# Performance work log

Measured on AMD Instinct MI355X. Metric: run time of the kernel, lower is better.

Reference implementation:

```python
import jax, jax.numpy as jnp
import numpy as np

B, T, D = 1, 8192, 1024
H, DH = 16, 64
WIN = 128          # attention window (tokens on each side)
WB = 128
NB = T // WB
EPS = 1e-5


def _layernorm(x, g, b):
    mu = jnp.mean(x, axis=-1, keepdims=True)
    var = jnp.mean(jnp.square(x - mu), axis=-1, keepdims=True)
    return (x - mu) * jax.lax.rsqrt(var + EPS) * g + b


def _band_mask():
    # query offset i in [0, WB), key offset j in [0, 3*WB) within [prev|self|next] blocks
    i = jnp.arange(WB)[:, None]
    j = jnp.arange(3 * WB)[None, :]
    rel = j - WB - i                      # key_pos - query_pos
    band = jnp.abs(rel) <= WIN            # sliding window |i-j| <= W (matches torch mask)
    blk = jnp.arange(NB)[:, None, None]
    key_pos = blk * WB + (j - WB)[None]   # absolute key position
    return band[None] & (key_pos >= 0) & (key_pos < T)   # [NB, WB, 3*WB]


def _local_attention(q, k, v):
    # q,k,v: [B,H,T,DH] -> block-local SDPA, mathematically identical to
    # full SDPA with the additive band mask in the torch code.
    def blocks(t):
        return t.reshape(B, H, NB, WB, DH)
    qb = blocks(q)
    kp = jnp.pad(blocks(k), ((0, 0), (0, 0), (1, 1), (0, 0), (0, 0)))
    vp = jnp.pad(blocks(v), ((0, 0), (0, 0), (1, 1), (0, 0), (0, 0)))
    # gather [prev, self, next] key/value blocks: [B,H,NB,3*WB,DH]
    k3 = jnp.concatenate([kp[:, :, s:s + NB] for s in range(3)], axis=3)
    v3 = jnp.concatenate([vp[:, :, s:s + NB] for s in range(3)], axis=3)
    scores = jnp.einsum('bhnqd,bhnkd->bhnqk', qb, k3) / np.sqrt(DH).astype(np.float32)
    mask = _band_mask()                                   # [NB,WB,3WB]
    scores = jnp.where(mask[None, None], scores, -jnp.inf)
    attn = jax.nn.softmax(scores, axis=-1)
    out = jnp.einsum('bhnqk,bhnkd->bhnqd', attn, v3)      # [B,H,NB,WB,DH]
    return out.reshape(B, H, T, DH)


def setup_inputs() -> dict:
    key = jax.random.key(0)
    ks = jax.random.split(key, 7)
    s = 0.02
    return {
        'x': jax.random.normal(ks[0], (B, T, D), jnp.float32),
        'wq': jax.random.normal(ks[1], (D, D), jnp.float32) * s,
        'wk': jax.random.normal(ks[2], (D, D), jnp.float32) * s,
        'wv': jax.random.normal(ks[3], (D, D), jnp.float32) * s,
        'wo': jax.random.normal(ks[4], (D, D), jnp.float32) * s,
        'wg': jax.random.normal(ks[5], (D, 2 * D), jnp.float32) * s,
        'wd': jax.random.normal(ks[6], (2 * D, D), jnp.float32) * s,
        'norm_g': jnp.ones((D,), jnp.float32),
        'norm_b': jnp.zeros((D,), jnp.float32),
        'ffn_g': jnp.ones((D,), jnp.float32),
        'ffn_b': jnp.zeros((D,), jnp.float32),
    }


def reference(x, wq, wk, wv, wo, wg, wd, norm_g, norm_b, ffn_g, ffn_b):
    h = _layernorm(x, norm_g, norm_b)
    def heads(t):  # [B,T,D] -> [B,H,T,DH]
        return t.reshape(B, T, H, DH).transpose(0, 2, 1, 3)
    q, k, v = heads(h @ wq), heads(h @ wk), heads(h @ wv)
    attn_out = _local_attention(q, k, v)                     # [B,H,T,DH]
    attn_out = attn_out.transpose(0, 2, 1, 3).reshape(B, T, D)
    x = x + attn_out @ wo
    h = _layernorm(x, ffn_g, ffn_b)
    x = x + jax.nn.silu(h @ wg) @ wd
    return x
```

## Files before the change

kernel.cpp:

```cpp
#include <hip/hip_runtime.h>
#include <cstdint>

#define T_DIM 8192
#define D_DIM 1024
#define NB_DIM 64
#define QKS 2048

typedef __bf16 bf16x8 __attribute__((ext_vector_type(8)));
typedef __bf16 bf16x4 __attribute__((ext_vector_type(4)));
typedef float f32x4 __attribute__((ext_vector_type(4)));

#define MFMA16(a, b, c) __builtin_amdgcn_mfma_f32_16x16x32_bf16((a), (b), (c), 0, 0, 0)
#define BAR() asm volatile("s_barrier" ::: "memory")
#define VMCNT(n) asm volatile("s_waitcnt vmcnt(" #n ")" ::: "memory")

__device__ __forceinline__ void gld_lds16(const void* gsrc, void* ldst) {
  __builtin_amdgcn_global_load_lds(
      (__attribute__((address_space(1))) void*)(uintptr_t)gsrc,
      (__attribute__((address_space(3))) void*)(uintptr_t)ldst,
      16, 0, 0);
}

__global__ __launch_bounds__(256) void prep_all(
    const float* __restrict__ wq, const float* __restrict__ wk,
    const float* __restrict__ wv, const float* __restrict__ wo,
    const float* __restrict__ wg, const float* __restrict__ wd,
    __bf16* __restrict__ wqkT, __bf16* __restrict__ wvT,
    __bf16* __restrict__ woT, __bf16* __restrict__ wgT,
    __bf16* __restrict__ wdT,
    const float* __restrict__ x, const float* __restrict__ ng,
    const float* __restrict__ nb, __bf16* __restrict__ h) {
  __shared__ float smem_f[32 * 33];
  const int bid = (int)blockIdx.x;
  const int tid = threadIdx.x;

  if (bid < 8192) {
    float (*tile)[33] = (float(*)[33])smem_f;
    const float* W; __bf16* Wt; int K, N, n0, k0, local;
    if (bid < 1024)      { W = wq; Wt = wqkT;            K = 1024; N = 1024; local = bid; }
    else if (bid < 2048) { W = wk; Wt = wqkT + 1048576;  K = 1024; N = 1024; local = bid - 1024; }
    else if (bid < 3072) { W = wv; Wt = wvT;             K = 1024; N = 1024; local = bid - 2048; }
    else if (bid < 4096) { W = wo; Wt = woT;             K = 1024; N = 1024; local = bid - 3072; }
    else if (bid < 6144) { W = wg; Wt = wgT;             K = 1024; N = 2048; local = bid - 4096; }
    else                 { W = wd; Wt = wdT;             K = 2048; N = 1024; local = bid - 6144; }
    if (N == 2048) { n0 = (local & 63) * 32; k0 = (local >> 6) * 32; }
    else           { n0 = (local & 31) * 32; k0 = (local >> 5) * 32; }
    const int tx = tid & 31, ty = tid >> 5;
#pragma unroll
    for (int i = 0; i < 32; i += 8)
      tile[ty + i][tx] = W[(size_t)(k0 + ty + i) * N + n0 + tx];
    __syncthreads();
#pragma unroll
    for (int i = 0; i < 32; i += 8)
      Wt[(size_t)(n0 + ty + i) * K + k0 + tx] = (__bf16)tile[tx][ty + i];
  } else {
    float* red = smem_f;
    const int row = bid - 8192;
    const float4 v = ((const float4*)(x + (size_t)row * D_DIM))[tid];
    float s = v.x + v.y + v.z + v.w;
#pragma unroll
    for (int off = 32; off >= 1; off >>= 1) s += __shfl_xor(s, off, 64);
    if ((tid & 63) == 0) red[tid >> 6] = s;
    __syncthreads();
    const float mean = (red[0] + red[1] + red[2] + red[3]) * (1.0f / D_DIM);
    const float d0 = v.x - mean, d1 = v.y - mean, d2 = v.z - mean, d3 = v.w - mean;
    float ss = d0 * d0 + d1 * d1 + d2 * d2 + d3 * d3;
#pragma unroll
    for (int off = 32; off >= 1; off >>= 1) ss += __shfl_xor(ss, off, 64);
    if ((tid & 63) == 0) red[4 + (tid >> 6)] = ss;
    __syncthreads();
    const float var = (red[4] + red[5] + red[6] + red[7]) * (1.0f / D_DIM);
    const float rstd = rsqrtf(var + 1e-5f);
    const float4 gg = ((const float4*)ng)[tid];
    const float4 bb = ((const float4*)nb)[tid];
    bf16x4 o;
    o[0] = (__bf16)(d0 * rstd * gg.x + bb.x);
    o[1] = (__bf16)(d1 * rstd * gg.y + bb.y);
    o[2] = (__bf16)(d2 * rstd * gg.z + bb.z);
    o[3] = (__bf16)(d3 * rstd * gg.w + bb.w);
    *(bf16x4*)(h + (size_t)row * D_DIM + tid * 4) = o;
  }
}

__global__ __launch_bounds__(256) void ln_kernel(
    const __bf16* __restrict__ x, const float* __restrict__ g,
    const float* __restrict__ b, __bf16* __restrict__ out) {
  __shared__ float red[8];
  const int row = blockIdx.x, tid = threadIdx.x;
  const bf16x4 v = ((const bf16x4*)(x + (size_t)row * D_DIM))[tid];
  const float v0 = (float)v[0], v1 = (float)v[1], v2 = (float)v[2], v3 = (float)v[3];
  float s = v0 + v1 + v2 + v3;
#pragma unroll
  for (int off = 32; off >= 1; off >>= 1) s += __shfl_xor(s, off, 64);
  if ((tid & 63) == 0) red[tid >> 6] = s;
  __syncthreads();
  const float mean = (red[0] + red[1] + red[2] + red[3]) * (1.0f / D_DIM);
  const float d0 = v0 - mean, d1 = v1 - mean, d2 = v2 - mean, d3 = v3 - mean;
  float ss = d0 * d0 + d1 * d1 + d2 * d2 + d3 * d3;
#pragma unroll
  for (int off = 32; off >= 1; off >>= 1) ss += __shfl_xor(ss, off, 64);
  if ((tid & 63) == 0) red[4 + (tid >> 6)] = ss;
  __syncthreads();
  const float var = (red[4] + red[5] + red[6] + red[7]) * (1.0f / D_DIM);
  const float rstd = rsqrtf(var + 1e-5f);
  const float4 gg = ((const float4*)g)[tid];
  const float4 bb = ((const float4*)b)[tid];
  bf16x4 o;
  o[0] = (__bf16)(d0 * rstd * gg.x + bb.x);
  o[1] = (__bf16)(d1 * rstd * gg.y + bb.y);
  o[2] = (__bf16)(d2 * rstd * gg.z + bb.z);
  o[3] = (__bf16)(d3 * rstd * gg.w + bb.w);
  *(bf16x4*)(out + (size_t)row * D_DIM + tid * 4) = o;
}

template <int BM_, int EPI, bool DUAL>
__global__ __launch_bounds__(512, 2) void gemm8(
    const __bf16* Ap, const __bf16* Btp, const void* Res, void* Coutp,
    int Mp, int Np, int K, int nbnp, int split,
    const __bf16* A2, const __bf16* Bt2, void* Cout2,
    int M2, int N2, int nbn2) {
  constexpr int MF = BM_ / 32;
  constexpr int MH = MF / 2;
  constexpr int SA = 8 * MF;
  constexpr int LA = BM_ / 128;
  constexpr int ATILE = BM_ * 64;
  constexpr int AHALF = BM_ * 32;
  constexpr int BOFF = 2 * ATILE;
  __shared__ __bf16 lds[2 * BM_ * 64 + 32768];

  const __bf16* A = Ap;
  const __bf16* Bt = Btp;
  void* Cout = Coutp;
  int M = Mp, N = Np, nbn = nbnp;
  int bid = (int)blockIdx.x;
  int nwg = gridDim.x;
  if constexpr (DUAL) {
    if (bid >= split) {
      A = A2; Bt = Bt2; Cout = Cout2; M = M2; N = N2; nbn = nbn2;
      bid -= split; nwg = gridDim.x - split;
    } else {
      nwg = split;
    }
  }
  (void)M;

  const int tid = threadIdx.x;
  const int l = tid & 63, w = tid >> 6;
  const int lr = l & 15, lg = l >> 4;
  const int wr = w >> 2, wc = w & 3;
  const int swz = (bid & 7) * (nwg >> 3) + (bid >> 3);
  const int bm = swz / nbn, bn = swz % nbn;
  const int am0 = bm * BM_, bn0 = bn * 256;

  f32x4 acc[MF][4];
  const f32x4 z4 = {0.f, 0.f, 0.f, 0.f};
#pragma unroll
  for (int m = 0; m < MF; ++m)
#pragma unroll
    for (int n = 0; n < 4; ++n) acc[m][n] = z4;

  auto stageA = [&](int h, int b, int k0) {
#pragma unroll
    for (int r = 0; r < LA; ++r) {
      const int ci = r * 512 + tid;
      const int wri = ci >> 3, c8 = ci & 7;
      const int ra = (wri % SA) + (wri / SA) * (2 * SA) + h * SA;
      gld_lds16(A + (size_t)(am0 + ra) * K + k0 + ((c8 ^ (wri & 7)) << 3),
                (__bf16*)lds + b * ATILE + h * AHALF + ci * 8);
    }
  };
  auto stageB = [&](int h, int b, int k0) {
#pragma unroll
    for (int r = 0; r < 2; ++r) {
      const int ci = r * 512 + tid;
      const int wri = ci >> 3, c8 = ci & 7;
      const int rb = (wri & 31) + (wri >> 5) * 64 + h * 32;
      gld_lds16(Bt + (size_t)(bn0 + rb) * K + k0 + ((c8 ^ (wri & 7)) << 3),
                (__bf16*)lds + BOFF + b * 16384 + h * 8192 + ci * 8);
    }
  };

  const int x7 = lr & 7;
  const int aoff0 = (lr + wr * SA) * 64 + ((lg) ^ x7) * 8;
  const int aoff1 = (lr + wr * SA) * 64 + ((4 + lg) ^ x7) * 8;
  const int boff0 = BOFF + (lr + wc * 32) * 64 + ((lg) ^ x7) * 8;
  const int boff1 = BOFF + (lr + wc * 32) * 64 + ((4 + lg) ^ x7) * 8;

  const int nt = K >> 6;
  stageA(0, 0, 0);
  stageB(1, 0, 0);
  stageB(0, 0, 0);
  stageA(1, 0, 0);
  stageA(0, 1, 64);
  stageB(1, 1, 64);
  if constexpr (BM_ == 256) VMCNT(6); else VMCNT(4);
  BAR();

  int buf = 0;
  bf16x8 afr[MH][2], bfr0[2][2], bfr1[2][2];
  for (int t = 0; t < nt; ++t) {
    const bool s1 = (t + 1 < nt);
    const bool s2 = (t + 2 < nt);
    const int nb_ = buf ^ 1;
    const int k1 = (t + 1) << 6;
    const int k2 = (t + 2) << 6;
    const __bf16* pa0 = lds + buf * ATILE + aoff0;
    const __bf16* pa1 = lds + buf * ATILE + aoff1;
    const __bf16* pb0 = lds + buf * 16384 + boff0;
    const __bf16* pb1 = lds + buf * 16384 + boff1;

#pragma unroll
    for (int i = 0; i < MH; ++i) {
      afr[i][0] = *(const bf16x8*)(pa0 + i * 1024);
      afr[i][1] = *(const bf16x8*)(pa1 + i * 1024);
    }
#pragma unroll
    for (int j = 0; j < 2; ++j) {
      bfr0[j][0] = *(const bf16x8*)(pb0 + j * 1024);
      bfr0[j][1] = *(const bf16x8*)(pb1 + j * 1024);
    }
    if (s1) stageB(0, nb_, k1);
    BAR();
    __builtin_amdgcn_s_setprio(1);
#pragma unroll
    for (int kk = 0; kk < 2; ++kk)
#pragma unroll
      for (int i = 0; i < MH; ++i)
#pragma unroll
        for (int j = 0; j < 2; ++j)
          acc[i][j] = MFMA16(afr[i][kk], bfr0[j][kk], acc[i][j]);
    __builtin_amdgcn_s_setprio(0);

#pragma unroll
    for (int j = 0; j < 2; ++j) {
      bfr1[j][0] = *(const bf16x8*)(pb0 + 8192 + j * 1024);
      bfr1[j][1] = *(const bf16x8*)(pb1 + 8192 + j * 1024);
    }
    if (s1) {
      stageA(1, nb_, k1);
      if constexpr (BM_ == 256) VMCNT(8); else VMCNT(6);
    } else {
      VMCNT(0);
    }
    BAR();
    __builtin_amdgcn_s_setprio(1);
#pragma unroll
    for (int kk = 0; kk < 2; ++kk)
#pragma unroll
      for (int i = 0; i < MH; ++i)
#pragma unroll
        for (int j = 0; j < 2; ++j)
          acc[i][2 + j] = MFMA16(afr[i][kk], bfr1[j][kk], acc[i][2 + j]);
    __builtin_amdgcn_s_setprio(0);

#pragma unroll
    for (int i = 0; i < MH; ++i) {
      afr[i][0] = *(const bf16x8*)(pa0 + AHALF + i * 1024);
      afr[i][1] = *(const bf16x8*)(pa1 + AHALF + i * 1024);
    }
    if (s2) stageA(0, buf, k2);
    BAR();
    __builtin_amdgcn_s_setprio(1);
#pragma unroll
    for (int kk = 0; kk < 2; ++kk)
#pragma unroll
      for (int i = 0; i < MH; ++i)
#pragma unroll
        for (int j = 0; j < 2; ++j)
          acc[MH + i][2 + j] = MFMA16(afr[i][kk], bfr1[j][kk], acc[MH + i][2 + j]);
    __builtin_amdgcn_s_setprio(0);

    if (s2) {
      stageB(1, buf, k2);
      if constexpr (BM_ == 256) VMCNT(6); else VMCNT(4);
    } else if (s1) {
      if constexpr (BM_ == 256) VMCNT(2); else VMCNT(1);
    }
    BAR();
    __builtin_amdgcn_s_setprio(1);
#pragma unroll
    for (int kk = 0; kk < 2; ++kk)
#pragma unroll
      for (int i = 0; i < MH; ++i)
#pragma unroll
        for (int j = 0; j < 2; ++j)
          acc[MH + i][j] = MFMA16(afr[i][kk], bfr0[j][kk], acc[MH + i][j]);
    __builtin_amdgcn_s_setprio(0);

    buf = nb_;
  }

  if constexpr (EPI == 5) {
    const __bf16* R = (const __bf16*)Res;
    float* O = (float*)Cout;
#pragma unroll
    for (int mf = 0; mf < MF; ++mf)
#pragma unroll
      for (int nf = 0; nf < 4; ++nf)
#pragma unroll
        for (int r = 0; r < 4; ++r) {
          const int row = am0 + wr * 2 * SA + mf * 16 + lg * 4 + r;
          const int col = bn0 + wc * 64 + nf * 16 + lr;
          const size_t idx = (size_t)row * N + col;
          O[idx] = acc[mf][nf][r] + (float)R[idx];
        }
  } else {
    __syncthreads();
    __bf16* Ct = (__bf16*)lds;
#pragma unroll
    for (int mf = 0; mf < MF; ++mf)
#pragma unroll
      for (int nf = 0; nf < 4; ++nf)
#pragma unroll
        for (int r = 0; r < 4; ++r) {
          const int rl = wr * 2 * SA + mf * 16 + lg * 4 + r;
          const int cl = wc * 64 + nf * 16 + lr;
          float v = acc[mf][nf][r];
          if constexpr (EPI == 3) v = v / (1.f + __expf(-v));
          if constexpr (EPI == 4)
            v += ((const float*)Res)[(size_t)(am0 + rl) * N + bn0 + cl];
          Ct[rl * 256 + (((cl >> 3) ^ (rl & 7)) << 3) + (cl & 7)] = (__bf16)v;
        }
    __syncthreads();
    __bf16* O = (__bf16*)Cout;
#pragma unroll
    for (int i = 0; i < BM_ / 16; ++i) {
      const int ci = i * 512 + tid;
      const int row = ci >> 5, c8 = ci & 31;
      *(bf16x8*)(O + (size_t)(am0 + row) * N + bn0 + c8 * 8) =
          *(const bf16x8*)&Ct[row * 256 + ((c8 ^ (row & 7)) << 3)];
    }
  }
}

template <int REL>
__device__ __forceinline__ void attn_tile(
    const __bf16* __restrict__ qk, const __bf16* __restrict__ vT,
    __bf16* Pw, const bf16x8 (&qf)[2][2], float (&ssum)[2][4],
    f32x4 (&o)[2][4], int kb, int h, int w, int lr, int lg) {
  const f32x4 z4 = {0.f, 0.f, 0.f, 0.f};
  const int kclo = (REL < 0) ? (w * 2) : 0;
  const int kchi = (REL > 0) ? (w * 2 + 2) : 8;

  f32x4 s[2][8];
  const __bf16* kbase = qk + (size_t)(kb * 128 + lr) * QKS + 1024 + h * 64 + lg * 8;
#pragma unroll
  for (int kc = 0; kc < 8; ++kc) {
    if (kc < kclo || kc >= kchi) continue;
    const bf16x8 k0 = *(const bf16x8*)(kbase + (size_t)kc * 16 * QKS);
    const bf16x8 k1 = *(const bf16x8*)(kbase + (size_t)kc * 16 * QKS + 32);
    s[0][kc] = MFMA16(qf[0][0], k0, z4);
    s[1][kc] = MFMA16(qf[1][0], k0, z4);
    s[0][kc] = MFMA16(qf[0][1], k1, s[0][kc]);
    s[1][kc] = MFMA16(qf[1][1], k1, s[1][kc]);
  }

#pragma unroll
  for (int m = 0; m < 2; ++m) {
#pragma unroll
    for (int r = 0; r < 4; ++r) {
      const int qi = w * 32 + m * 16 + lg * 4 + r;
      float acc_s = 0.f;
#pragma unroll
      for (int kc = 0; kc < 8; ++kc) {
        if (kc < kclo || kc >= kchi) continue;
        const int kj = kc * 16 + lr;
        float p = __expf(s[m][kc][r] * 0.125f);
        const bool valid = (REL == 0) || (REL < 0 ? (kj >= qi) : (kj <= qi));
        p = valid ? p : 0.f;
        s[m][kc][r] = p;
        acc_s += p;
      }
      ssum[m][r] += acc_s;
    }
  }

#pragma unroll
  for (int m = 0; m < 2; ++m)
#pragma unroll
    for (int kc = 0; kc < 8; ++kc) {
      if (kc < kclo || kc >= kchi) continue;
#pragma unroll
      for (int r = 0; r < 4; ++r)
        Pw[(m * 16 + lg * 4 + r) * 136 + kc * 16 + lr] = (__bf16)s[m][kc][r];
    }

  const int kslo = kclo >> 1, kshi = kchi >> 1;
  const __bf16* vbase = vT + (size_t)(h * 64 + lr) * T_DIM + kb * 128 + lg * 8;
#pragma unroll
  for (int ks = 0; ks < 4; ++ks) {
    if (ks < kslo || ks >= kshi) continue;
    bf16x8 pa[2];
#pragma unroll
    for (int m = 0; m < 2; ++m)
      pa[m] = *(const bf16x8*)&Pw[(m * 16 + lr) * 136 + ks * 32 + lg * 8];
#pragma unroll
    for (int n = 0; n < 4; ++n) {
      const bf16x8 vb = *(const bf16x8*)(vbase + (size_t)n * 16 * T_DIM + ks * 32);
      o[0][n] = MFMA16(pa[0], vb, o[0][n]);
      o[1][n] = MFMA16(pa[1], vb, o[1][n]);
    }
  }
}

__global__ __launch_bounds__(64, 2) void attn_kernel(
    const __bf16* __restrict__ qk, const __bf16* __restrict__ vT,
    __bf16* __restrict__ out) {
  __shared__ __bf16 Pw[32 * 136];

  const int l = (int)threadIdx.x;
  const int lr = l & 15, lg = l >> 4;
  const int bx = (int)blockIdx.x;
  const int swz = (bx & 7) * 512 + (bx >> 3);
  const int h = swz >> 8;
  const int blk = (swz >> 2) & 63;
  const int w = swz & 3;

  const __bf16* qbase =
      qk + (size_t)(blk * 128 + w * 32 + lr) * QKS + h * 64 + lg * 8;
  bf16x8 qf[2][2];
#pragma unroll
  for (int m = 0; m < 2; ++m)
#pragma unroll
    for (int ks = 0; ks < 2; ++ks)
      qf[m][ks] = *(const bf16x8*)(qbase + (size_t)m * 16 * QKS + ks * 32);

  bf16x8 kf0[8][2];
  {
    const __bf16* kbase =
        qk + (size_t)(blk * 128 + lr) * QKS + 1024 + h * 64 + lg * 8;
#pragma unroll
    for (int kc = 0; kc < 8; ++kc) {
      kf0[kc][0] = *(const bf16x8*)(kbase + (size_t)kc * 16 * QKS);
      kf0[kc][1] = *(const bf16x8*)(kbase + (size_t)kc * 16 * QKS + 32);
    }
  }

  const f32x4 z4 = {0.f, 0.f, 0.f, 0.f};
  float ssum[2][4];
  f32x4 o[2][4];
#pragma unroll
  for (int m = 0; m < 2; ++m) {
#pragma unroll
    for (int r = 0; r < 4; ++r) ssum[m][r] = 0.f;
#pragma unroll
    for (int n = 0; n < 4; ++n) o[m][n] = z4;
  }

  {
    f32x4 s[2][8];
#pragma unroll
    for (int kc = 0; kc < 8; ++kc) {
      s[0][kc] = MFMA16(qf[0][0], kf0[kc][0], z4);
      s[1][kc] = MFMA16(qf[1][0], kf0[kc][0], z4);
      s[0][kc] = MFMA16(qf[0][1], kf0[kc][1], s[0][kc]);
      s[1][kc] = MFMA16(qf[1][1], kf0[kc][1], s[1][kc]);
    }
#pragma unroll
    for (int m = 0; m < 2; ++m)
#pragma unroll
      for (int r = 0; r < 4; ++r) {
        float acc_s = 0.f;
#pragma unroll
        for (int kc = 0; kc < 8; ++kc) {
          const float p = __expf(s[m][kc][r] * 0.125f);
          s[m][kc][r] = p;
          acc_s += p;
        }
        ssum[m][r] += acc_s;
      }
#pragma unroll
    for (int m = 0; m < 2; ++m)
#pragma unroll
      for (int kc = 0; kc < 8; ++kc)
#pragma unroll
        for (int r = 0; r < 4; ++r)
          Pw[(m * 16 + lg * 4 + r) * 136 + kc * 16 + lr] = (__bf16)s[m][kc][r];
    const __bf16* vbase =
        vT + (size_t)(h * 64 + lr) * T_DIM + blk * 128 + lg * 8;
#pragma unroll
    for (int ks = 0; ks < 4; ++ks) {
      bf16x8 pa[2];
#pragma unroll
      for (int m = 0; m < 2; ++m)
        pa[m] = *(const bf16x8*)&Pw[(m * 16 + lr) * 136 + ks * 32 + lg * 8];
#pragma unroll
      for (int n = 0; n < 4; ++n) {
        const bf16x8 vb = *(const bf16x8*)(vbase + (size_t)n * 16 * T_DIM + ks * 32);
        o[0][n] = MFMA16(pa[0], vb, o[0][n]);
        o[1][n] = MFMA16(pa[1], vb, o[1][n]);
      }
    }
  }

  if (blk > 0)
    attn_tile<-1>(qk, vT, Pw, qf, ssum, o, blk - 1, h, w, lr, lg);
  if (blk < NB_DIM - 1)
    attn_tile<1>(qk, vT, Pw, qf, ssum, o, blk + 1, h, w, lr, lg);

  float inv[2][4];
#pragma unroll
  for (int m = 0; m < 2; ++m)
#pragma unroll
    for (int r = 0; r < 4; ++r) {
      float rs = ssum[m][r];
#pragma unroll
      for (int off = 1; off < 16; off <<= 1) rs += __shfl_xor(rs, off, 64);
      inv[m][r] = __builtin_amdgcn_rcpf(rs);
    }
#pragma unroll
  for (int m = 0; m < 2; ++m)
#pragma unroll
    for (int n = 0; n < 4; ++n)
#pragma unroll
      for (int r = 0; r < 4; ++r)
        Pw[(m * 16 + lg * 4 + r) * 136 + n * 16 + lr] =
            (__bf16)(o[m][n][r] * inv[m][r]);
#pragma unroll
  for (int i = 0; i < 4; ++i) {
    const int ci = i * 64 + l;
    const int qrow = ci >> 3;
    const int c8 = (ci & 7) * 8;
    const bf16x8 vv = *(const bf16x8*)&Pw[qrow * 136 + c8];
    *(bf16x8*)(out + (size_t)(blk * 128 + w * 32 + qrow) * D_DIM + h * 64 + c8) = vv;
  }
}

extern "C" void kernel_launch(void* const* d_in, const int* in_sizes, int n_in,
                              void* d_out, int out_size, void* d_ws, size_t ws_size,
                              hipStream_t stream) {
  (void)in_sizes; (void)n_in; (void)out_size; (void)ws_size;
  const float* x      = (const float*)d_in[0];
  const float* wq     = (const float*)d_in[1];
  const float* wk     = (const float*)d_in[2];
  const float* wv     = (const float*)d_in[3];
  const float* wo     = (const float*)d_in[4];
  const float* wg     = (const float*)d_in[5];
  const float* wd     = (const float*)d_in[6];
  const float* norm_g = (const float*)d_in[7];
  const float* norm_b = (const float*)d_in[8];
  const float* ffn_g  = (const float*)d_in[9];
  const float* ffn_b  = (const float*)d_in[10];
  float* out = (float*)d_out;

  char* ws = (char*)d_ws;
  constexpr size_t MB = 1ull << 20;
  __bf16* wqkT = (__bf16*)(ws + 0 * MB);
  __bf16* wvT  = (__bf16*)(ws + 4 * MB);
  __bf16* woT  = (__bf16*)(ws + 6 * MB);
  __bf16* wgT  = (__bf16*)(ws + 8 * MB);
  __bf16* wdT  = (__bf16*)(ws + 12 * MB);
  __bf16* hbuf = (__bf16*)(ws + 16 * MB);
  __bf16* qkbf = (__bf16*)(ws + 32 * MB);
  __bf16* gbf  = (__bf16*)(ws + 32 * MB);
  __bf16* vTbf = (__bf16*)(ws + 64 * MB);
  __bf16* x2bf = (__bf16*)(ws + 80 * MB);

  prep_all<<<16384, 256, 0, stream>>>(wq, wk, wv, wo, wg, wd,
                                      wqkT, wvT, woT, wgT, wdT,
                                      x, norm_g, norm_b, hbuf);

  gemm8<128, 0, true><<<768, 512, 0, stream>>>(
      hbuf, wqkT, nullptr, qkbf, 8192, 2048, 1024, 8, 512,
      wvT, hbuf, vTbf, 1024, 8192, 32);

  attn_kernel<<<4096, 64, 0, stream>>>(qkbf, vTbf, hbuf);

  gemm8<128, 4, false><<<256, 512, 0, stream>>>(
      hbuf, woT, x, x2bf, 8192, 1024, 1024, 4, 0,
      nullptr, nullptr, nullptr, 0, 0, 1);

  ln_kernel<<<8192, 256, 0, stream>>>(x2bf, ffn_g, ffn_b, hbuf);

  gemm8<256, 3, false><<<256, 512, 0, stream>>>(
      hbuf, wgT, nullptr, gbf, 8192, 2048, 1024, 8, 0,
      nullptr, nullptr, nullptr, 0, 0, 1);

  gemm8<128, 5, false><<<256, 512, 0, stream>>>(
      gbf, wdT, x2bf, out, 8192, 1024, 2048, 4, 0,
      nullptr, nullptr, nullptr, 0, 0, 1);
}
```

Measured before the change: 232.6 us.

## Split attention work into 16-query-row wavefronts and double grid size

```diff
diff --git a/kernel.cpp b/kernel.cpp
--- a/kernel.cpp
+++ b/kernel.cpp
@@ -334,96 +334,83 @@
 }
 
 template <int REL>
-__device__ __forceinline__ void attn_tile(
+__device__ __forceinline__ void attn_tile16(
     const __bf16* __restrict__ qk, const __bf16* __restrict__ vT,
-    __bf16* Pw, const bf16x8 (&qf)[2][2], float (&ssum)[2][4],
-    f32x4 (&o)[2][4], int kb, int h, int w, int lr, int lg) {
+    __bf16* Pw, const bf16x8 (&qf)[2], float (&ssum)[4],
+    f32x4 (&o)[4], int kb, int h, int w8, int lr, int lg) {
   const f32x4 z4 = {0.f, 0.f, 0.f, 0.f};
-  const int kclo = (REL < 0) ? (w * 2) : 0;
-  const int kchi = (REL > 0) ? (w * 2 + 2) : 8;
-
-  f32x4 s[2][8];
+  const int kclo = (REL < 0) ? w8 : 0;
+  const int kchi = (REL > 0) ? (w8 + 1) : 8;
+
+  f32x4 s[8];
   const __bf16* kbase = qk + (size_t)(kb * 128 + lr) * QKS + 1024 + h * 64 + lg * 8;
 #pragma unroll
   for (int kc = 0; kc < 8; ++kc) {
     if (kc < kclo || kc >= kchi) continue;
     const bf16x8 k0 = *(const bf16x8*)(kbase + (size_t)kc * 16 * QKS);
     const bf16x8 k1 = *(const bf16x8*)(kbase + (size_t)kc * 16 * QKS + 32);
-    s[0][kc] = MFMA16(qf[0][0], k0, z4);
-    s[1][kc] = MFMA16(qf[1][0], k0, z4);
-    s[0][kc] = MFMA16(qf[0][1], k1, s[0][kc]);
-    s[1][kc] = MFMA16(qf[1][1], k1, s[1][kc]);
-  }
-
-#pragma unroll
-  for (int m = 0; m < 2; ++m) {
-#pragma unroll
-    for (int r = 0; r < 4; ++r) {
-      const int qi = w * 32 + m * 16 + lg * 4 + r;
-      float acc_s = 0.f;
-#pragma unroll
-      for (int kc = 0; kc < 8; ++kc) {
-        if (kc < kclo || kc >= kchi) continue;
-        const int kj = kc * 16 + lr;
-        float p = __expf(s[m][kc][r] * 0.125f);
-        const bool valid = (REL == 0) || (REL < 0 ? (kj >= qi) : (kj <= qi));
-        p = valid ? p : 0.f;
-        s[m][kc][r] = p;
-        acc_s += p;
-      }
-      ssum[m][r] += acc_s;
-    }
-  }
-
-#pragma unroll
-  for (int m = 0; m < 2; ++m)
+    s[kc] = MFMA16(qf[0], k0, z4);
+    s[kc] = MFMA16(qf[1], k1, s[kc]);
+  }
+
+#pragma unroll
+  for (int r = 0; r < 4; ++r) {
+    const int qi = w8 * 16 + lg * 4 + r;
+    float acc_s = 0.f;
 #pragma unroll
     for (int kc = 0; kc < 8; ++kc) {
       if (kc < kclo || kc >= kchi) continue;
-#pragma unroll
-      for (int r = 0; r < 4; ++r)
-        Pw[(m * 16 + lg * 4 + r) * 136 + kc * 16 + lr] = (__bf16)s[m][kc][r];
-    }
-
-  const int kslo = kclo >> 1, kshi = kchi >> 1;
+      const int kj = kc * 16 + lr;
+      float p = __expf(s[kc][r] * 0.125f);
+      const bool valid = (REL < 0) ? (kj >= qi) : (kj <= qi);
+      p = valid ? p : 0.f;
+      s[kc][r] = p;
+      acc_s += p;
+    }
+    ssum[r] += acc_s;
+  }
+
+#pragma unroll
+  for (int kc = 0; kc < 8; ++kc) {
+    if (kc < kclo || kc >= kchi) continue;
+#pragma unroll
+    for (int r = 0; r < 4; ++r)
+      Pw[(lg * 4 + r) * 136 + kc * 16 + lr] = (__bf16)s[kc][r];
+  }
+
+  const int kslo = kclo >> 1;
+  const int kshi = ((kchi - 1) >> 1) + 1;
   const __bf16* vbase = vT + (size_t)(h * 64 + lr) * T_DIM + kb * 128 + lg * 8;
 #pragma unroll
   for (int ks = 0; ks < 4; ++ks) {
     if (ks < kslo || ks >= kshi) continue;
-    bf16x8 pa[2];
-#pragma unroll
-    for (int m = 0; m < 2; ++m)
-      pa[m] = *(const bf16x8*)&Pw[(m * 16 + lr) * 136 + ks * 32 + lg * 8];
+    const bf16x8 pa = *(const bf16x8*)&Pw[lr * 136 + ks * 32 + lg * 8];
 #pragma unroll
     for (int n = 0; n < 4; ++n) {
       const bf16x8 vb = *(const bf16x8*)(vbase + (size_t)n * 16 * T_DIM + ks * 32);
-      o[0][n] = MFMA16(pa[0], vb, o[0][n]);
-      o[1][n] = MFMA16(pa[1], vb, o[1][n]);
-    }
-  }
-}
-
-__global__ __launch_bounds__(64, 2) void attn_kernel(
+      o[n] = MFMA16(pa, vb, o[n]);
+    }
+  }
+}
+
+__global__ __launch_bounds__(64, 4) void attn_kernel(
     const __bf16* __restrict__ qk, const __bf16* __restrict__ vT,
     __bf16* __restrict__ out) {
-  __shared__ __bf16 Pw[32 * 136];
+  __shared__ __bf16 Pw[16 * 136];
 
   const int l = (int)threadIdx.x;
   const int lr = l & 15, lg = l >> 4;
   const int bx = (int)blockIdx.x;
-  const int swz = (bx & 7) * 512 + (bx >> 3);
-  const int h = swz >> 8;
-  const int blk = (swz >> 2) & 63;
-  const int w = swz & 3;
+  const int swz = (bx & 7) * 1024 + (bx >> 3);
+  const int h = swz >> 9;
+  const int blk = (swz >> 3) & 63;
+  const int w8 = swz & 7;
 
   const __bf16* qbase =
-      qk + (size_t)(blk * 128 + w * 32 + lr) * QKS + h * 64 + lg * 8;
-  bf16x8 qf[2][2];
-#pragma unroll
-  for (int m = 0; m < 2; ++m)
-#pragma unroll
-    for (int ks = 0; ks < 2; ++ks)
-      qf[m][ks] = *(const bf16x8*)(qbase + (size_t)m * 16 * QKS + ks * 32);
+      qk + (size_t)(blk * 128 + w8 * 16 + lr) * QKS + h * 64 + lg * 8;
+  bf16x8 qf[2];
+  qf[0] = *(const bf16x8*)(qbase);
+  qf[1] = *(const bf16x8*)(qbase + 32);
 
   bf16x8 kf0[8][2];
   {
@@ -437,92 +424,74 @@
   }
 
   const f32x4 z4 = {0.f, 0.f, 0.f, 0.f};
-  float ssum[2][4];
-  f32x4 o[2][4];
-#pragma unroll
-  for (int m = 0; m < 2; ++m) {
-#pragma unroll
-    for (int r = 0; r < 4; ++r) ssum[m][r] = 0.f;
-#pragma unroll
-    for (int n = 0; n < 4; ++n) o[m][n] = z4;
-  }
+  float ssum[4];
+  f32x4 o[4];
+#pragma unroll
+  for (int r = 0; r < 4; ++r) ssum[r] = 0.f;
+#pragma unroll
+  for (int n = 0; n < 4; ++n) o[n] = z4;
 
   {
-    f32x4 s[2][8];
+    f32x4 s[8];
 #pragma unroll
     for (int kc = 0; kc < 8; ++kc) {
-      s[0][kc] = MFMA16(qf[0][0], kf0[kc][0], z4);
-      s[1][kc] = MFMA16(qf[1][0], kf0[kc][0], z4);
-      s[0][kc] = MFMA16(qf[0][1], kf0[kc][1], s[0][kc]);
-      s[1][kc] = MFMA16(qf[1][1], kf0[kc][1], s[1][kc]);
-    }
-#pragma unroll
-    for (int m = 0; m < 2; ++m)
-#pragma unroll
-      for (int r = 0; r < 4; ++r) {
-        float acc_s = 0.f;
-#pragma unroll
-        for (int kc = 0; kc < 8; ++kc) {
-          const float p = __expf(s[m][kc][r] * 0.125f);
-          s[m][kc][r] = p;
-          acc_s += p;
-        }
-        ssum[m][r] += acc_s;
+      s[kc] = MFMA16(qf[0], kf0[kc][0], z4);
+      s[kc] = MFMA16(qf[1], kf0[kc][1], s[kc]);
+    }
+#pragma unroll
+    for (int r = 0; r < 4; ++r) {
+      float acc_s = 0.f;
+#pragma unroll
+      for (int kc = 0; kc < 8; ++kc) {
+        const float p = __expf(s[kc][r] * 0.125f);
+        s[kc][r] = p;
+        acc_s += p;
       }
-#pragma unroll
-    for (int m = 0; m < 2; ++m)
-#pragma unroll
-      for (int kc = 0; kc < 8; ++kc)
-#pragma unroll
-        for (int r = 0; r < 4; ++r)
-          Pw[(m * 16 + lg * 4 + r) * 136 + kc * 16 + lr] = (__bf16)s[m][kc][r];
+      ssum[r] += acc_s;
+    }
+#pragma unroll
+    for (int kc = 0; kc < 8; ++kc)
+#pragma unroll
+      for (int r = 0; r < 4; ++r)
+        Pw[(lg * 4 + r) * 136 + kc * 16 + lr] = (__bf16)s[kc][r];
     const __bf16* vbase =
         vT + (size_t)(h * 64 + lr) * T_DIM + blk * 128 + lg * 8;
 #pragma unroll
     for (int ks = 0; ks < 4; ++ks) {
-      bf16x8 pa[2];
-#pragma unroll
-      for (int m = 0; m < 2; ++m)
-        pa[m] = *(const bf16x8*)&Pw[(m * 16 + lr) * 136 + ks * 32 + lg * 8];
+      const bf16x8 pa = *(const bf16x8*)&Pw[lr * 136 + ks * 32 + lg * 8];
 #pragma unroll
       for (int n = 0; n < 4; ++n) {
         const bf16x8 vb = *(const bf16x8*)(vbase + (size_t)n * 16 * T_DIM + ks * 32);
-        o[0][n] = MFMA16(pa[0], vb, o[0][n]);
-        o[1][n] = MFMA16(pa[1], vb, o[1][n]);
+        o[n] = MFMA16(pa, vb, o[n]);
       }
     }
   }
 
   if (blk > 0)
-    attn_tile<-1>(qk, vT, Pw, qf, ssum, o, blk - 1, h, w, lr, lg);
+    attn_tile16<-1>(qk, vT, Pw, qf, ssum, o, blk - 1, h, w8, lr, lg);
   if (blk < NB_DIM - 1)
-    attn_tile<1>(qk, vT, Pw, qf, ssum, o, blk + 1, h, w, lr, lg);
-
-  float inv[2][4];
-#pragma unroll
-  for (int m = 0; m < 2; ++m)
-#pragma unroll
-    for (int r = 0; r < 4; ++r) {
-      float rs = ssum[m][r];
-#pragma unroll
-      for (int off = 1; off < 16; off <<= 1) rs += __shfl_xor(rs, off, 64);
-      inv[m][r] = __builtin_amdgcn_rcpf(rs);
-    }
-#pragma unroll
-  for (int m = 0; m < 2; ++m)
-#pragma unroll
-    for (int n = 0; n < 4; ++n)
-#pragma unroll
-      for (int r = 0; r < 4; ++r)
-        Pw[(m * 16 + lg * 4 + r) * 136 + n * 16 + lr] =
-            (__bf16)(o[m][n][r] * inv[m][r]);
-#pragma unroll
-  for (int i = 0; i < 4; ++i) {
+    attn_tile16<1>(qk, vT, Pw, qf, ssum, o, blk + 1, h, w8, lr, lg);
+
+  float inv[4];
+#pragma unroll
+  for (int r = 0; r < 4; ++r) {
+    float rs = ssum[r];
+#pragma unroll
+    for (int off = 1; off < 16; off <<= 1) rs += __shfl_xor(rs, off, 64);
+    inv[r] = __builtin_amdgcn_rcpf(rs);
+  }
+#pragma unroll
+  for (int n = 0; n < 4; ++n)
+#pragma unroll
+    for (int r = 0; r < 4; ++r)
+      Pw[(lg * 4 + r) * 136 + n * 16 + lr] = (__bf16)(o[n][r] * inv[r]);
+#pragma unroll
+  for (int i = 0; i < 2; ++i) {
     const int ci = i * 64 + l;
     const int qrow = ci >> 3;
     const int c8 = (ci & 7) * 8;
     const bf16x8 vv = *(const bf16x8*)&Pw[qrow * 136 + c8];
-    *(bf16x8*)(out + (size_t)(blk * 128 + w * 32 + qrow) * D_DIM + h * 64 + c8) = vv;
+    *(bf16x8*)(out + (size_t)(blk * 128 + w8 * 16 + qrow) * D_DIM + h * 64 + c8) = vv;
   }
 }
 
@@ -564,7 +533,7 @@
       hbuf, wqkT, nullptr, qkbf, 8192, 2048, 1024, 8, 512,
       wvT, hbuf, vTbf, 1024, 8192, 32);
 
-  attn_kernel<<<4096, 64, 0, stream>>>(qkbf, vTbf, hbuf);
+  attn_kernel<<<8192, 64, 0, stream>>>(qkbf, vTbf, hbuf);
 
   gemm8<128, 4, false><<<256, 512, 0, stream>>>(
       hbuf, woT, x, x2bf, 8192, 1024, 1024, 4, 0,
```

After: 290.3 us. +24.8%, slower.
